# Optimization experiments

Measured on AMD Instinct MI355X. Metric: run time of the kernel, lower is better.

The kernel has to match this reference:

```python
import jax, jax.numpy as jnp
import numpy as np

N_NODES = 50000
N_EDGES = 500000
D_IN = 128
HID = 128
OUT = 2
N_REL = 4
BN_EPS = 1e-5


def setup_inputs() -> dict:
    key = jax.random.key(0)
    ks = jax.random.split(key, 14)
    s_in = 1.0 / np.sqrt(D_IN)
    s_h = 1.0 / np.sqrt(HID)
    return {
        "x": jax.random.normal(ks[0], (N_NODES, D_IN), jnp.float32),
        "edge_index": jax.random.randint(ks[1], (N_REL, 2, N_EDGES), 0, N_NODES, jnp.int32),
        "W1": jax.random.normal(ks[2], (N_REL, D_IN, HID), jnp.float32) * s_in,
        "b1": jax.random.normal(ks[3], (N_REL, HID), jnp.float32) * s_in,
        "W2": jax.random.normal(ks[4], (N_REL, HID, HID), jnp.float32) * s_h,
        "b2": jax.random.normal(ks[5], (N_REL, HID), jnp.float32) * s_h,
        "bn_gamma": jnp.ones((HID,), jnp.float32),
        "bn_beta": jnp.zeros((HID,), jnp.float32),
        "lin1_W": jax.random.normal(ks[6], (HID, HID), jnp.float32) * s_h,
        "lin1_b": jax.random.normal(ks[7], (HID,), jnp.float32) * s_h,
        "lin2_W": jax.random.normal(ks[8], (HID, OUT), jnp.float32) * s_h,
        "lin2_b": jax.random.normal(ks[9], (OUT,), jnp.float32) * s_h,
    }


def _gcn(x, ei, W, b):
    # GCNConv: D^-1/2 (A + I) D^-1/2 (X W) + b
    n = x.shape[0]
    h = x @ W                                    # [N, H]
    loops = jnp.arange(n, dtype=ei.dtype)
    src = jnp.concatenate([ei[0], loops])        # add self loops
    dst = jnp.concatenate([ei[1], loops])
    deg = jax.ops.segment_sum(jnp.ones(dst.shape, h.dtype), dst, num_segments=n)
    dinv = jnp.where(deg > 0, jax.lax.rsqrt(deg), 0.0)
    norm = dinv[src] * dinv[dst]                 # [E+N]
    msg = h[src] * norm[:, None]                 # gather + scale
    return jax.ops.segment_sum(msg, dst, num_segments=n) + b


def _hetero(x, edge_index, W, b):
    # HeteroConv with aggr='sum' over the 4 relation types (same src/dst node type)
    out = _gcn(x, edge_index[0], W[0], b[0])
    for r in range(1, N_REL):
        out = out + _gcn(x, edge_index[r], W[r], b[r])
    return out


def reference(x, edge_index, W1, b1, W2, b2, bn_gamma, bn_beta, lin1_W, lin1_b, lin2_W, lin2_b):
    h = jax.nn.relu(_hetero(x, edge_index, W1, b1))
    h = jax.nn.relu(_hetero(h, edge_index, W2, b2))
    # BatchNorm1d (batch statistics, biased variance)
    mean = h.mean(axis=0)
    var = h.var(axis=0)
    h = (h - mean) * jax.lax.rsqrt(var + BN_EPS) * bn_gamma + bn_beta
    h = jax.nn.relu(h @ lin1_W + lin1_b)
    # dropout is identity in eval
    return h @ lin2_W + lin2_b
```

## Files before the change

### kernel.cpp

```cpp
#include <hip/hip_runtime.h>
#include <math.h>

#define NN 50000
#define NE 500000
#define NREL 4
#define D 128
#define RSZ 512
#define NRANGE 98
#define NBK (NREL * NRANGE)
#define BCAP 6144
#define NCH 128
#define CH 3907
#define FCAP 96
#define CAST_BLKS 6250
#define BINBLKS (NCH * NREL)
static constexpr float BN_EPS = 1e-5f;

typedef __attribute__((ext_vector_type(8))) _Float16 half8;
typedef __attribute__((ext_vector_type(4))) float f32x4;

__device__ __forceinline__ unsigned short f2h_bits(float f) {
    _Float16 h = (_Float16)f;
    return __builtin_bit_cast(unsigned short, h);
}
__device__ __forceinline__ float hi2f(unsigned p) {
    return (float)__builtin_bit_cast(_Float16, (unsigned short)(p >> 16));
}

__global__ __launch_bounds__(256) void k_prebin(const float* __restrict__ x,
                                                const float* __restrict__ W1, const float* __restrict__ W2,
                                                const float* __restrict__ l1W, const float* __restrict__ b1,
                                                const float* __restrict__ b2,
                                                unsigned short* __restrict__ xb,
                                                unsigned short* __restrict__ Wt1,
                                                unsigned short* __restrict__ Wt2,
                                                unsigned short* __restrict__ Wt3,
                                                float* __restrict__ bs1, float* __restrict__ bs2,
                                                float* __restrict__ bnsum,
                                                const int* __restrict__ ei,
                                                int* __restrict__ frag,
                                                int* __restrict__ cntg) {
    __shared__ int bins[NRANGE * FCAP];
    __shared__ int cnt[NRANGE];
    int tid = threadIdx.x;
    if (blockIdx.x < BINBLKS) {
        int c = blockIdx.x & (NCH - 1), r = blockIdx.x >> 7;
        const int* srcp = ei + r * 2 * NE;
        const int* dstp = srcp + NE;
        for (int i = tid; i < NRANGE; i += 256) cnt[i] = 0;
        __syncthreads();
        int e0 = c * CH, e1 = min(e0 + CH, NE);
        for (int e = e0 + tid; e < e1; e += 256) {
            int d = dstp[e];
            int s = srcp[e];
            int q = d >> 9;
            int pos = atomicAdd(&cnt[q], 1);
            if (pos < FCAP) bins[q * FCAP + pos] = s | ((d & 511) << 16);
        }
        __syncthreads();
        int w = tid >> 6, lane = tid & 63;
        for (int q = w; q < NRANGE; q += 4) {
            int k = min(cnt[q], FCAP);
            int gbase = ((r * NRANGE + q) * NCH + c) * FCAP;
            for (int i = lane; i < k; i += 64) frag[gbase + i] = bins[q * FCAP + i];
        }
        for (int q = tid; q < NRANGE; q += 256) cntg[(r * NRANGE + q) * NCH + c] = min(cnt[q], FCAP);
        return;
    }
    int blk = blockIdx.x - BINBLKS;
    if (blk < CAST_BLKS) {
        int i = blk * 256 + tid;
        float4 v = *(const float4*)(x + (size_t)i * 4);
        unsigned short u[4] = {f2h_bits(v.x), f2h_bits(v.y), f2h_bits(v.z), f2h_bits(v.w)};
        *(ushort4*)(xb + (size_t)i * 4) = *(ushort4*)u;
    } else if (blk < CAST_BLKS + 256) {
        int i = (blk - CAST_BLKS) * 256 + tid;
        int kk = i & 511, n = i >> 9;
        Wt1[n * 512 + kk] = f2h_bits(W1[kk * 128 + n]);
        Wt2[n * 512 + kk] = f2h_bits(W2[kk * 128 + n]);
    } else if (blk < CAST_BLKS + 320) {
        int i = (blk - CAST_BLKS - 256) * 256 + tid;
        int kk = i & 127, n = i >> 7;
        Wt3[n * 128 + kk] = f2h_bits(l1W[kk * 128 + n]);
    } else {
        if (tid < 128) {
            bs1[tid] = b1[tid] + b1[128 + tid] + b1[256 + tid] + b1[384 + tid];
            bs2[tid] = b2[tid] + b2[128 + tid] + b2[256 + tid] + b2[384 + tid];
        }
        bnsum[tid] = 0.f;
    }
}

__global__ __launch_bounds__(512) void k_sortb(const int* __restrict__ frag,
                                               const int* __restrict__ cntg,
                                               unsigned short* __restrict__ csr,
                                               int* __restrict__ rstart,
                                               int* __restrict__ rend,
                                               float* __restrict__ dinv) {
    int q = blockIdx.x, r = blockIdx.y;
    int blk = r * NRANGE + q;
    int n0 = q * RSZ;
    int nrows = min(RSZ, NN - n0);
    __shared__ int cnts[NCH], cbase[NCH];
    __shared__ int stage[BCAP];
    __shared__ unsigned short csr_s[BCAP];
    __shared__ int hist[RSZ], off[RSZ], cnt2[RSZ];
    int tid = threadIdx.x;
    hist[tid] = 0;
    cnt2[tid] = 0;
    if (tid < NCH) cnts[tid] = cntg[blk * NCH + tid];
    __syncthreads();
    if (tid < NCH) cbase[tid] = cnts[tid];
    __syncthreads();
    for (int d = 1; d < NCH; d <<= 1) {
        int t = 0;
        if (tid < NCH && tid >= d) t = cbase[tid - d];
        __syncthreads();
        if (tid < NCH) cbase[tid] += t;
        __syncthreads();
    }
    if (tid < NCH) cbase[tid] -= cnts[tid];
    __syncthreads();
    int tot = cbase[NCH - 1] + cnts[NCH - 1];
    {
        int g = tid >> 2, l = tid & 3;
        int k = cnts[g], cb = cbase[g];
        int gbase = (blk * NCH + g) * FCAP;
        for (int i = l; i < k; i += 4)
            if (cb + i < BCAP) stage[cb + i] = frag[gbase + i];
    }
    __syncthreads();
    if (tot > BCAP) tot = BCAP;
    for (int i = tid; i < tot; i += 512) atomicAdd(&hist[(stage[i] >> 16) & 511], 1);
    __syncthreads();
    int h = hist[tid];
    if (tid < nrows) dinv[r * NN + n0 + tid] = rsqrtf((float)(h + 1));
    off[tid] = h;
    __syncthreads();
    for (int d = 1; d < RSZ; d <<= 1) {
        int t = (tid >= d) ? off[tid - d] : 0;
        __syncthreads();
        off[tid] += t;
        __syncthreads();
    }
    int excl = off[tid] - h;
    __syncthreads();
    off[tid] = excl;
    int base = blk * BCAP;
    if (tid < nrows) {
        rstart[r * NN + n0 + tid] = base + excl;
        rend[r * NN + n0 + tid] = base + excl + h;
    }
    __syncthreads();
    for (int i = tid; i < tot; i += 512) {
        int v = stage[i];
        int dl = (v >> 16) & 511;
        int p = atomicAdd(&cnt2[dl], 1);
        csr_s[off[dl] + p] = (unsigned short)(v & 0xFFFF);
    }
    __syncthreads();
    for (int i = tid; i < tot; i += 512) csr[base + i] = csr_s[i];
}

__global__ __launch_bounds__(256) void k_wei(const unsigned short* __restrict__ csr,
                                             const float* __restrict__ dinv,
                                             unsigned* __restrict__ wpack) {
    int gi = blockIdx.x * 256 + threadIdx.x;
    int r = gi / (NRANGE * BCAP);
    int s = csr[gi];
    float w = dinv[r * NN + min(s, NN - 1)];
    wpack[gi] = (unsigned)s | ((unsigned)f2h_bits(w) << 16);
}

__global__ __launch_bounds__(256) void k_agg(const unsigned short* __restrict__ in,
                                             const unsigned* __restrict__ wpack,
                                             const int* __restrict__ rstart,
                                             const int* __restrict__ rend,
                                             const float* __restrict__ dinv,
                                             unsigned short* __restrict__ Acat) {
    int wave = threadIdx.x >> 6, lane = threadIdx.x & 63;
    int n = blockIdx.x * 4 + wave;
    if (n >= NN) return;
    int t = lane & 15;
    int base = lane & 48;
    int nb = (base >> 4) * NN + n;
    const half8* in8 = (const half8*)in;
    float wn = dinv[nb];
    int start = rstart[nb];
    int deg = rend[nb] - start;
    int dm = deg;
    dm = max(dm, __shfl_xor(dm, 16));
    dm = max(dm, __shfl_xor(dm, 32));
    half8 us = in8[(size_t)n * 16 + t];
    float a[8];
#pragma unroll
    for (int j = 0; j < 8; j++) a[j] = wn * (float)us[j];

    for (int w0 = 0; w0 < dm; w0 += 16) {
        int li = w0 + t;
        int gi = min(start + li, NBK * BCAP - 1);
        unsigned pv = wpack[gi];
        if (li >= deg) pv = 0u;
        unsigned p0 = __shfl(pv, base + 0), p1 = __shfl(pv, base + 1);
        unsigned p2 = __shfl(pv, base + 2), p3 = __shfl(pv, base + 3);
        unsigned p4 = __shfl(pv, base + 4), p5 = __shfl(pv, base + 5);
        unsigned p6 = __shfl(pv, base + 6), p7 = __shfl(pv, base + 7);
        {
            half8 r0 = in8[(p0 & 0xFFFFu) * 16 + t];
            half8 r1 = in8[(p1 & 0xFFFFu) * 16 + t];
            half8 r2 = in8[(p2 & 0xFFFFu) * 16 + t];
            half8 r3 = in8[(p3 & 0xFFFFu) * 16 + t];
            half8 r4 = in8[(p4 & 0xFFFFu) * 16 + t];
            half8 r5 = in8[(p5 & 0xFFFFu) * 16 + t];
            half8 r6 = in8[(p6 & 0xFFFFu) * 16 + t];
            half8 r7 = in8[(p7 & 0xFFFFu) * 16 + t];
            float w0f = hi2f(p0), w1f = hi2f(p1), w2f = hi2f(p2), w3f = hi2f(p3);
            float w4f = hi2f(p4), w5f = hi2f(p5), w6f = hi2f(p6), w7f = hi2f(p7);
#pragma unroll
            for (int j = 0; j < 8; j++) a[j] = fmaf((float)r0[j], w0f, a[j]);
#pragma unroll
            for (int j = 0; j < 8; j++) a[j] = fmaf((float)r1[j], w1f, a[j]);
#pragma unroll
            for (int j = 0; j < 8; j++) a[j] = fmaf((float)r2[j], w2f, a[j]);
#pragma unroll
            for (int j = 0; j < 8; j++) a[j] = fmaf((float)r3[j], w3f, a[j]);
#pragma unroll
            for (int j = 0; j < 8; j++) a[j] = fmaf((float)r4[j], w4f, a[j]);
#pragma unroll
            for (int j = 0; j < 8; j++) a[j] = fmaf((float)r5[j], w5f, a[j]);
#pragma unroll
            for (int j = 0; j < 8; j++) a[j] = fmaf((float)r6[j], w6f, a[j]);
#pragma unroll
            for (int j = 0; j < 8; j++) a[j] = fmaf((float)r7[j], w7f, a[j]);
        }
        if (w0 + 8 >= dm) continue;
        p0 = __shfl(pv, base + 8);  p1 = __shfl(pv, base + 9);
        p2 = __shfl(pv, base + 10); p3 = __shfl(pv, base + 11);
        p4 = __shfl(pv, base + 12); p5 = __shfl(pv, base + 13);
        p6 = __shfl(pv, base + 14); p7 = __shfl(pv, base + 15);
        {
            half8 r0 = in8[(p0 & 0xFFFFu) * 16 + t];
            half8 r1 = in8[(p1 & 0xFFFFu) * 16 + t];
            half8 r2 = in8[(p2 & 0xFFFFu) * 16 + t];
            half8 r3 = in8[(p3 & 0xFFFFu) * 16 + t];
            half8 r4 = in8[(p4 & 0xFFFFu) * 16 + t];
            half8 r5 = in8[(p5 & 0xFFFFu) * 16 + t];
            half8 r6 = in8[(p6 & 0xFFFFu) * 16 + t];
            half8 r7 = in8[(p7 & 0xFFFFu) * 16 + t];
            float w0f = hi2f(p0), w1f = hi2f(p1), w2f = hi2f(p2), w3f = hi2f(p3);
            float w4f = hi2f(p4), w5f = hi2f(p5), w6f = hi2f(p6), w7f = hi2f(p7);
#pragma unroll
            for (int j = 0; j < 8; j++) a[j] = fmaf((float)r0[j], w0f, a[j]);
#pragma unroll
            for (int j = 0; j < 8; j++) a[j] = fmaf((float)r1[j], w1f, a[j]);
#pragma unroll
            for (int j = 0; j < 8; j++) a[j] = fmaf((float)r2[j], w2f, a[j]);
#pragma unroll
            for (int j = 0; j < 8; j++) a[j] = fmaf((float)r3[j], w3f, a[j]);
#pragma unroll
            for (int j = 0; j < 8; j++) a[j] = fmaf((float)r4[j], w4f, a[j]);
#pragma unroll
            for (int j = 0; j < 8; j++) a[j] = fmaf((float)r5[j], w5f, a[j]);
#pragma unroll
            for (int j = 0; j < 8; j++) a[j] = fmaf((float)r6[j], w6f, a[j]);
#pragma unroll
            for (int j = 0; j < 8; j++) a[j] = fmaf((float)r7[j], w7f, a[j]);
        }
    }
    _Float16 ob[8];
#pragma unroll
    for (int j = 0; j < 8; j++) ob[j] = (_Float16)(wn * a[j]);
    *(half8*)(Acat + (size_t)n * 512 + (base << 3) + t * 8) = *(half8*)ob;
}

template <bool STATS>
__global__ __launch_bounds__(512, 2) void k_mm(const unsigned short* __restrict__ A,
                                               const unsigned short* __restrict__ Bt,
                                               const float* __restrict__ bias,
                                               unsigned short* __restrict__ C,
                                               float* __restrict__ bnsum) {
    constexpr int LDP = 524;
    __shared__ unsigned short wl[128 * LDP];
    int tid = threadIdx.x;
    int wave = tid >> 6, lane = tid & 63;
    int ln = lane & 15, quad = lane >> 4;
    int b0 = blockIdx.x * 200;
    int m0 = b0 + wave * 32;
    int mEnd = b0 + 200;
    size_t arow0 = (size_t)min(m0 + ln, NN - 1) * 512;
    size_t arow1 = (size_t)min(m0 + 16 + ln, NN - 1) * 512;

    half8 a0v[16], a1v[16];
#pragma unroll
    for (int ks = 0; ks < 16; ++ks) {
        int kof = ks * 32 + quad * 8;
        a0v[ks] = *(const half8*)(A + arow0 + kof);
        a1v[ks] = *(const half8*)(A + arow1 + kof);
    }
#pragma unroll
    for (int i = 0; i < 16; ++i) {
        int h = tid + i * 512;
        int col = h >> 6;
        int k = (h & 63) * 8;
        *(half8*)(wl + col * LDP + k) = *(const half8*)(Bt + (size_t)h * 8);
    }
    __syncthreads();

    f32x4 acc[2][8];
#pragma unroll
    for (int a = 0; a < 2; a++)
#pragma unroll
        for (int b = 0; b < 8; b++) acc[a][b] = (f32x4){0.f, 0.f, 0.f, 0.f};

#pragma unroll
    for (int ks = 0; ks < 16; ++ks) {
        int kof = ks * 32 + quad * 8;
#pragma unroll
        for (int nf = 0; nf < 8; nf++) {
            half8 bf = *(const half8*)(wl + (nf * 16 + ln) * LDP + kof);
            acc[0][nf] = __builtin_amdgcn_mfma_f32_16x16x32_f16(a0v[ks], bf, acc[0][nf], 0, 0, 0);
            acc[1][nf] = __builtin_amdgcn_mfma_f32_16x16x32_f16(a1v[ks], bf, acc[1][nf], 0, 0, 0);
        }
    }

    float bs[8];
#pragma unroll
    for (int nf = 0; nf < 8; nf++) bs[nf] = bias[nf * 16 + ln];
    float sn[8], qn[8];
#pragma unroll
    for (int nf = 0; nf < 8; nf++) { sn[nf] = 0.f; qn[nf] = 0.f; }

#pragma unroll
    for (int mf = 0; mf < 2; mf++)
#pragma unroll
        for (int nf = 0; nf < 8; nf++)
#pragma unroll
            for (int rg = 0; rg < 4; rg++) {
                int m = m0 + mf * 16 + quad * 4 + rg;
                if (m < mEnd && m < NN) {
                    float v = fmaxf(acc[mf][nf][rg] + bs[nf], 0.f);
                    if (STATS) { sn[nf] += v; qn[nf] += v * v; }
                    C[(size_t)m * 128 + nf * 16 + ln] = f2h_bits(v);
                }
            }

    if (STATS) {
#pragma unroll
        for (int nf = 0; nf < 8; nf++) {
            float s = sn[nf], q = qn[nf];
            s += __shfl_xor(s, 16); s += __shfl_xor(s, 32);
            q += __shfl_xor(q, 16); q += __shfl_xor(q, 32);
            if (quad == 0) {
                unsafeAtomicAdd(&bnsum[nf * 16 + ln], s);
                unsafeAtomicAdd(&bnsum[128 + nf * 16 + ln], q);
            }
        }
    }
}

__global__ __launch_bounds__(256) void k_final(const unsigned short* __restrict__ R2,
                                               const float* __restrict__ bnsum,
                                               const float* __restrict__ gamma,
                                               const float* __restrict__ beta,
                                               const unsigned short* __restrict__ Wt3,
                                               const float* __restrict__ l1b,
                                               const float* __restrict__ l2W,
                                               const float* __restrict__ l2b,
                                               float* __restrict__ out) {
    __shared__ float bnp_s[256];
    __shared__ unsigned short wl[128 * 136];
    int tid = threadIdx.x;
    if (tid < 128) {
        float mean = bnsum[tid] / (float)NN;
        float var = bnsum[128 + tid] / (float)NN - mean * mean;
        float sc = gamma[tid] * rsqrtf(var + BN_EPS);
        bnp_s[tid] = sc;
        bnp_s[128 + tid] = beta[tid] - mean * sc;
    }
    {
        int col = tid >> 1, s = tid & 1;
        const unsigned short* gp = Wt3 + (size_t)col * 128 + s * 64;
        unsigned short* lp = wl + col * 136 + s * 64;
#pragma unroll
        for (int i = 0; i < 8; i++) *(half8*)(lp + i * 8) = *(const half8*)(gp + i * 8);
    }
    int w = tid >> 6, lane = tid & 63;
    int ln = lane & 15, quad = lane >> 4;
    int m0 = blockIdx.x * 64 + w * 16;
    size_t arow = (size_t)min(m0 + ln, NN - 1) * 128;
    half8 rv[4];
#pragma unroll
    for (int ks = 0; ks < 4; ks++) rv[ks] = *(const half8*)(R2 + arow + ks * 32 + quad * 8);
    __syncthreads();

    f32x4 acc[8];
#pragma unroll
    for (int b = 0; b < 8; b++) acc[b] = (f32x4){0.f, 0.f, 0.f, 0.f};

#pragma unroll
    for (int ks = 0; ks < 4; ks++) {
        int kof = ks * 32 + quad * 8;
        _Float16 ab[8];
#pragma unroll
        for (int j = 0; j < 8; j++)
            ab[j] = (_Float16)(fmaf((float)rv[ks][j], bnp_s[kof + j], bnp_s[128 + kof + j]));
        half8 af = *(half8*)ab;
#pragma unroll
        for (int nf = 0; nf < 8; nf++) {
            half8 bf = *(const half8*)(wl + (nf * 16 + ln) * 136 + kof);
            acc[nf] = __builtin_amdgcn_mfma_f32_16x16x32_f16(af, bf, acc[nf], 0, 0, 0);
        }
    }

    float b1v[8], w0[8], w1[8];
#pragma unroll
    for (int nf = 0; nf < 8; nf++) {
        int n = nf * 16 + ln;
        b1v[nf] = l1b[n];
        w0[nf] = l2W[n * 2];
        w1[nf] = l2W[n * 2 + 1];
    }
    float ob0 = l2b[0], ob1 = l2b[1];
#pragma unroll
    for (int rg = 0; rg < 4; rg++) {
        float p0 = 0.f, p1 = 0.f;
#pragma unroll
        for (int nf = 0; nf < 8; nf++) {
            float y = fmaxf(acc[nf][rg] + b1v[nf], 0.f);
            p0 += y * w0[nf];
            p1 += y * w1[nf];
        }
        p0 += __shfl_xor(p0, 1); p0 += __shfl_xor(p0, 2);
        p0 += __shfl_xor(p0, 4); p0 += __shfl_xor(p0, 8);
        p1 += __shfl_xor(p1, 1); p1 += __shfl_xor(p1, 2);
        p1 += __shfl_xor(p1, 4); p1 += __shfl_xor(p1, 8);
        int m = m0 + quad * 4 + rg;
        if (ln == 0 && m < NN) {
            out[(size_t)m * 2 + 0] = p0 + ob0;
            out[(size_t)m * 2 + 1] = p1 + ob1;
        }
    }
}

extern "C" void kernel_launch(void* const* d_in, const int* in_sizes, int n_in,
                              void* d_out, int out_size, void* d_ws, size_t ws_size,
                              hipStream_t stream) {
    const float* x = (const float*)d_in[0];
    const int* ei = (const int*)d_in[1];
    const float* W1 = (const float*)d_in[2];
    const float* b1 = (const float*)d_in[3];
    const float* W2 = (const float*)d_in[4];
    const float* b2 = (const float*)d_in[5];
    const float* gamma = (const float*)d_in[6];
    const float* beta = (const float*)d_in[7];
    const float* l1W = (const float*)d_in[8];
    const float* l1b = (const float*)d_in[9];
    const float* l2W = (const float*)d_in[10];
    const float* l2b = (const float*)d_in[11];
    float* out = (float*)d_out;

    char* ws = (char*)d_ws;
    size_t off = 0;
    auto alloc = [&](size_t bytes) {
        void* p = ws + off;
        off += (bytes + 255) & ~(size_t)255;
        return p;
    };
    float* dinv = (float*)alloc((size_t)NREL * NN * sizeof(float));
    int* rstart = (int*)alloc((size_t)NREL * NN * sizeof(int));
    int* rend = (int*)alloc((size_t)NREL * NN * sizeof(int));
    unsigned short* csr = (unsigned short*)alloc((size_t)NBK * BCAP * 2);
    unsigned* wpack = (unsigned*)alloc((size_t)NBK * BCAP * 4);
    unsigned short* xb = (unsigned short*)alloc((size_t)NN * D * 2);
    unsigned short* Acat = (unsigned short*)alloc((size_t)NN * 512 * 2);
    unsigned short* h1b = (unsigned short*)alloc((size_t)NN * D * 2);
    unsigned short* R2b = (unsigned short*)alloc((size_t)NN * D * 2);
    unsigned short* Wt1 = (unsigned short*)alloc(128 * 512 * 2);
    unsigned short* Wt2 = (unsigned short*)alloc(128 * 512 * 2);
    unsigned short* Wt3 = (unsigned short*)alloc(128 * 128 * 2);
    float* bs1 = (float*)alloc(128 * sizeof(float));
    float* bs2 = (float*)alloc(128 * sizeof(float));
    float* bnsum = (float*)alloc(256 * sizeof(float));

    int* frag = (int*)Acat;
    int* cntg = frag + (size_t)NREL * NRANGE * NCH * FCAP;

    k_prebin<<<BINBLKS + CAST_BLKS + 321, 256, 0, stream>>>(x, W1, W2, l1W, b1, b2, xb,
                                                            Wt1, Wt2, Wt3, bs1, bs2, bnsum,
                                                            ei, frag, cntg);
    dim3 sgrid(NRANGE, NREL);
    k_sortb<<<sgrid, 512, 0, stream>>>(frag, cntg, csr, rstart, rend, dinv);
    k_wei<<<(NBK * BCAP) / 256, 256, 0, stream>>>(csr, dinv, wpack);

    int agrid = (NN + 3) / 4;
    int mgrid = 250;
    int fgrid = (NN + 63) / 64;
    k_agg<<<agrid, 256, 0, stream>>>(xb, wpack, rstart, rend, dinv, Acat);
    k_mm<false><<<mgrid, 512, 0, stream>>>(Acat, Wt1, bs1, h1b, nullptr);
    k_agg<<<agrid, 256, 0, stream>>>(h1b, wpack, rstart, rend, dinv, Acat);
    k_mm<true><<<mgrid, 512, 0, stream>>>(Acat, Wt2, bs2, R2b, bnsum);
    k_final<<<fgrid, 256, 0, stream>>>(R2b, bnsum, gamma, beta, Wt3, l1b, l2W, l2b, out);
}
```

Baseline: 360.6 us.

## Restructure dense GEMM into double-buffered K-tiles with direct global-to-LDS loads

The fused [N,512]x[512,128] GEMM kernel now uses 64-row blocks of 256 threads instead of 200-row blocks of 512 threads. It walks K in 8 tiles of 64, double-buffering A and B tiles in LDS with XOR-swizzled layouts. Tiles are loaded with global_load_lds so the next tile streams in while MFMAs run on the current one. This replaces the old scheme, which held the whole A row slice in registers and staged the full weight matrix in LDS, aiming to cut register and LDS pressure, raise occupancy and overlap loads with compute. In exchange, every block re-reads the weight tiles and the kernel runs more blocks and barriers.

Result: slower. 400.7 us (+11.1%).

```diff
diff --git a/kernel.cpp b/kernel.cpp
--- a/kernel.cpp
+++ b/kernel.cpp
@@ -25,6 +25,11 @@
 }
 __device__ __forceinline__ float hi2f(unsigned p) {
     return (float)__builtin_bit_cast(_Float16, (unsigned short)(p >> 16));
+}
+__device__ __forceinline__ void gload_lds16(const void* g, void* l) {
+    __builtin_amdgcn_global_load_lds(
+        (const __attribute__((address_space(1))) void*)g,
+        (__attribute__((address_space(3))) void*)l, 16, 0, 0);
 }
 
 __global__ __launch_bounds__(256) void k_prebin(const float* __restrict__ x,
@@ -274,52 +279,59 @@
 }
 
 template <bool STATS>
-__global__ __launch_bounds__(512, 2) void k_mm(const unsigned short* __restrict__ A,
-                                               const unsigned short* __restrict__ Bt,
-                                               const float* __restrict__ bias,
-                                               unsigned short* __restrict__ C,
-                                               float* __restrict__ bnsum) {
-    constexpr int LDP = 524;
-    __shared__ unsigned short wl[128 * LDP];
+__global__ __launch_bounds__(256) void k_mm(const unsigned short* __restrict__ A,
+                                            const unsigned short* __restrict__ Bt,
+                                            const float* __restrict__ bias,
+                                            unsigned short* __restrict__ C,
+                                            float* __restrict__ bnsum) {
+    __shared__ unsigned short As[2][64 * 64];
+    __shared__ unsigned short Bs[2][128 * 64];
     int tid = threadIdx.x;
-    int wave = tid >> 6, lane = tid & 63;
+    int w = tid >> 6, lane = tid & 63;
     int ln = lane & 15, quad = lane >> 4;
-    int b0 = blockIdx.x * 200;
-    int m0 = b0 + wave * 32;
-    int mEnd = b0 + 200;
-    size_t arow0 = (size_t)min(m0 + ln, NN - 1) * 512;
-    size_t arow1 = (size_t)min(m0 + 16 + ln, NN - 1) * 512;
-
-    half8 a0v[16], a1v[16];
-#pragma unroll
-    for (int ks = 0; ks < 16; ++ks) {
-        int kof = ks * 32 + quad * 8;
-        a0v[ks] = *(const half8*)(A + arow0 + kof);
-        a1v[ks] = *(const half8*)(A + arow1 + kof);
-    }
-#pragma unroll
-    for (int i = 0; i < 16; ++i) {
-        int h = tid + i * 512;
-        int col = h >> 6;
-        int k = (h & 63) * 8;
-        *(half8*)(wl + col * LDP + k) = *(const half8*)(Bt + (size_t)h * 8);
-    }
-    __syncthreads();
-
-    f32x4 acc[2][8];
-#pragma unroll
-    for (int a = 0; a < 2; a++)
-#pragma unroll
-        for (int b = 0; b < 8; b++) acc[a][b] = (f32x4){0.f, 0.f, 0.f, 0.f};
-
-#pragma unroll
-    for (int ks = 0; ks < 16; ++ks) {
-        int kof = ks * 32 + quad * 8;
-#pragma unroll
-        for (int nf = 0; nf < 8; nf++) {
-            half8 bf = *(const half8*)(wl + (nf * 16 + ln) * LDP + kof);
-            acc[0][nf] = __builtin_amdgcn_mfma_f32_16x16x32_f16(a0v[ks], bf, acc[0][nf], 0, 0, 0);
-            acc[1][nf] = __builtin_amdgcn_mfma_f32_16x16x32_f16(a1v[ks], bf, acc[1][nf], 0, 0, 0);
+    int bm0 = blockIdx.x * 64;
+
+    auto stage = [&](int buf, int t) {
+        size_t kb = (size_t)t * 128;
+#pragma unroll
+        for (int s = 0; s < 2; ++s) {
+            int c = (s * 4 + w) * 64 + lane;
+            int row = c >> 3;
+            int gb = ((c & 7) << 4) ^ ((row & 7) << 4);
+            const char* gp = (const char*)A + (size_t)min(bm0 + row, NN - 1) * 1024 + kb + gb;
+            gload_lds16(gp, (char*)As[buf] + (s * 4 + w) * 1024);
+        }
+#pragma unroll
+        for (int s = 0; s < 4; ++s) {
+            int c = (s * 4 + w) * 64 + lane;
+            int col = c >> 3;
+            int gb = ((c & 7) << 4) ^ ((col & 7) << 4);
+            const char* gp = (const char*)Bt + (size_t)col * 1024 + kb + gb;
+            gload_lds16(gp, (char*)Bs[buf] + (s * 4 + w) * 1024);
+        }
+    };
+
+    stage(0, 0);
+
+    f32x4 acc[8];
+#pragma unroll
+    for (int b = 0; b < 8; b++) acc[b] = (f32x4){0.f, 0.f, 0.f, 0.f};
+
+    int swz = (ln & 7) << 4;
+#pragma unroll
+    for (int t = 0; t < 8; ++t) {
+        int cur = t & 1;
+        __syncthreads();
+        if (t < 7) stage(cur ^ 1, t + 1);
+#pragma unroll
+        for (int kk = 0; kk < 2; ++kk) {
+            int b0 = (kk * 64 + quad * 16) ^ swz;
+            half8 af = *(const half8*)((const char*)As[cur] + (w * 16 + ln) * 128 + b0);
+#pragma unroll
+            for (int nf = 0; nf < 8; nf++) {
+                half8 bf = *(const half8*)((const char*)Bs[cur] + (nf * 16 + ln) * 128 + b0);
+                acc[nf] = __builtin_amdgcn_mfma_f32_16x16x32_f16(af, bf, acc[nf], 0, 0, 0);
+            }
         }
     }
 
@@ -330,19 +342,18 @@
 #pragma unroll
     for (int nf = 0; nf < 8; nf++) { sn[nf] = 0.f; qn[nf] = 0.f; }
 
-#pragma unroll
-    for (int mf = 0; mf < 2; mf++)
-#pragma unroll
-        for (int nf = 0; nf < 8; nf++)
-#pragma unroll
-            for (int rg = 0; rg < 4; rg++) {
-                int m = m0 + mf * 16 + quad * 4 + rg;
-                if (m < mEnd && m < NN) {
-                    float v = fmaxf(acc[mf][nf][rg] + bs[nf], 0.f);
-                    if (STATS) { sn[nf] += v; qn[nf] += v * v; }
-                    C[(size_t)m * 128 + nf * 16 + ln] = f2h_bits(v);
-                }
+    int mw = bm0 + w * 16;
+#pragma unroll
+    for (int nf = 0; nf < 8; nf++)
+#pragma unroll
+        for (int rg = 0; rg < 4; rg++) {
+            int m = mw + quad * 4 + rg;
+            if (m < NN) {
+                float v = fmaxf(acc[nf][rg] + bs[nf], 0.f);
+                if (STATS) { sn[nf] += v; qn[nf] += v * v; }
+                C[(size_t)m * 128 + nf * 16 + ln] = f2h_bits(v);
             }
+        }
 
     if (STATS) {
 #pragma unroll
@@ -493,11 +504,11 @@
     k_wei<<<(NBK * BCAP) / 256, 256, 0, stream>>>(csr, dinv, wpack);
 
     int agrid = (NN + 3) / 4;
-    int mgrid = 250;
+    int mgrid = (NN + 63) / 64;
     int fgrid = (NN + 63) / 64;
     k_agg<<<agrid, 256, 0, stream>>>(xb, wpack, rstart, rend, dinv, Acat);
-    k_mm<false><<<mgrid, 512, 0, stream>>>(Acat, Wt1, bs1, h1b, nullptr);
+    k_mm<false><<<mgrid, 256, 0, stream>>>(Acat, Wt1, bs1, h1b, nullptr);
     k_agg<<<agrid, 256, 0, stream>>>(h1b, wpack, rstart, rend, dinv, Acat);
-    k_mm<true><<<mgrid, 512, 0, stream>>>(Acat, Wt2, bs2, R2b, bnsum);
+    k_mm<true><<<mgrid, 256, 0, stream>>>(Acat, Wt2, bs2, R2b, bnsum);
     k_final<<<fgrid, 256, 0, stream>>>(R2b, bnsum, gamma, beta, Wt3, l1b, l2W, l2b, out);
 }
```

## Stream GEMM operands from global memory instead of staging weights in LDS

Applied to the files above, without the earlier changes.

The k_mm GEMM no longer stages the 128x512 half weight matrix in LDS and no longer preloads the full A rows into registers. Each wave now reads A and B fragments straight from global memory (relying on L2/cache for B reuse) in a k-loop. Blocks shrink to 256 threads covering 128 rows, so the grid grows to about 391 blocks. This removes the roughly 134KB LDS footprint and the register pressure, which should allow more occupancy, but B is re-fetched per wave from cache rather than from LDS.

New measurement: 384.9 us. 1.07x slower.

```diff
diff --git a/kernel.cpp b/kernel.cpp
--- a/kernel.cpp
+++ b/kernel.cpp
@@ -274,37 +274,15 @@
 }
 
 template <bool STATS>
-__global__ __launch_bounds__(512, 2) void k_mm(const unsigned short* __restrict__ A,
+__global__ __launch_bounds__(256, 2) void k_mm(const unsigned short* __restrict__ A,
                                                const unsigned short* __restrict__ Bt,
                                                const float* __restrict__ bias,
                                                unsigned short* __restrict__ C,
                                                float* __restrict__ bnsum) {
-    constexpr int LDP = 524;
-    __shared__ unsigned short wl[128 * LDP];
     int tid = threadIdx.x;
-    int wave = tid >> 6, lane = tid & 63;
+    int w = tid >> 6, lane = tid & 63;
     int ln = lane & 15, quad = lane >> 4;
-    int b0 = blockIdx.x * 200;
-    int m0 = b0 + wave * 32;
-    int mEnd = b0 + 200;
-    size_t arow0 = (size_t)min(m0 + ln, NN - 1) * 512;
-    size_t arow1 = (size_t)min(m0 + 16 + ln, NN - 1) * 512;
-
-    half8 a0v[16], a1v[16];
-#pragma unroll
-    for (int ks = 0; ks < 16; ++ks) {
-        int kof = ks * 32 + quad * 8;
-        a0v[ks] = *(const half8*)(A + arow0 + kof);
-        a1v[ks] = *(const half8*)(A + arow1 + kof);
-    }
-#pragma unroll
-    for (int i = 0; i < 16; ++i) {
-        int h = tid + i * 512;
-        int col = h >> 6;
-        int k = (h & 63) * 8;
-        *(half8*)(wl + col * LDP + k) = *(const half8*)(Bt + (size_t)h * 8);
-    }
-    __syncthreads();
+    int m0 = blockIdx.x * 128 + w * 32;
 
     f32x4 acc[2][8];
 #pragma unroll
@@ -312,15 +290,28 @@
 #pragma unroll
         for (int b = 0; b < 8; b++) acc[a][b] = (f32x4){0.f, 0.f, 0.f, 0.f};
 
-#pragma unroll
-    for (int ks = 0; ks < 16; ++ks) {
-        int kof = ks * 32 + quad * 8;
-#pragma unroll
-        for (int nf = 0; nf < 8; nf++) {
-            half8 bf = *(const half8*)(wl + (nf * 16 + ln) * LDP + kof);
-            acc[0][nf] = __builtin_amdgcn_mfma_f32_16x16x32_f16(a0v[ks], bf, acc[0][nf], 0, 0, 0);
-            acc[1][nf] = __builtin_amdgcn_mfma_f32_16x16x32_f16(a1v[ks], bf, acc[1][nf], 0, 0, 0);
-        }
+    size_t arow[2];
+#pragma unroll
+    for (int mf = 0; mf < 2; mf++) {
+        int m = m0 + mf * 16 + ln;
+        arow[mf] = (size_t)min(m, NN - 1) * 512;
+    }
+    size_t brow[8];
+#pragma unroll
+    for (int nf = 0; nf < 8; nf++) brow[nf] = (size_t)(nf * 16 + ln) * 512;
+
+    for (int k0 = 0; k0 < 512; k0 += 32) {
+        int kof = k0 + quad * 8;
+        half8 af[2], bf[8];
+#pragma unroll
+        for (int mf = 0; mf < 2; mf++) af[mf] = *(const half8*)(A + arow[mf] + kof);
+#pragma unroll
+        for (int nf = 0; nf < 8; nf++) bf[nf] = *(const half8*)(Bt + brow[nf] + kof);
+#pragma unroll
+        for (int mf = 0; mf < 2; mf++)
+#pragma unroll
+            for (int nf = 0; nf < 8; nf++)
+                acc[mf][nf] = __builtin_amdgcn_mfma_f32_16x16x32_f16(af[mf], bf[nf], acc[mf][nf], 0, 0, 0);
     }
 
     float bs[8];
@@ -337,7 +328,7 @@
 #pragma unroll
             for (int rg = 0; rg < 4; rg++) {
                 int m = m0 + mf * 16 + quad * 4 + rg;
-                if (m < mEnd && m < NN) {
+                if (m < NN) {
                     float v = fmaxf(acc[mf][nf][rg] + bs[nf], 0.f);
                     if (STATS) { sn[nf] += v; qn[nf] += v * v; }
                     C[(size_t)m * 128 + nf * 16 + ln] = f2h_bits(v);
@@ -493,11 +484,11 @@
     k_wei<<<(NBK * BCAP) / 256, 256, 0, stream>>>(csr, dinv, wpack);
 
     int agrid = (NN + 3) / 4;
-    int mgrid = 250;
+    int mgrid = (NN + 127) / 128;
     int fgrid = (NN + 63) / 64;
     k_agg<<<agrid, 256, 0, stream>>>(xb, wpack, rstart, rend, dinv, Acat);
-    k_mm<false><<<mgrid, 512, 0, stream>>>(Acat, Wt1, bs1, h1b, nullptr);
+    k_mm<false><<<mgrid, 256, 0, stream>>>(Acat, Wt1, bs1, h1b, nullptr);
     k_agg<<<agrid, 256, 0, stream>>>(h1b, wpack, rstart, rend, dinv, Acat);
-    k_mm<true><<<mgrid, 512, 0, stream>>>(Acat, Wt2, bs2, R2b, bnsum);
+    k_mm<true><<<mgrid, 256, 0, stream>>>(Acat, Wt2, bs2, R2b, bnsum);
     k_final<<<fgrid, 256, 0, stream>>>(R2b, bnsum, gamma, beta, Wt3, l1b, l2W, l2b, out);
 }
```
